# Kernel optimization log

Hardware: AMD Instinct MI355X
Metric: run time of the kernel (lower is better)

The kernel has to match this reference:

```python
import jax, jax.numpy as jnp
import numpy as np

N_NODES = 100000

def gcn_conv(x, edge_index, W, b):
    # normalize=False GCNConv: out[i] = sum_{(j->i) in E} (x W)[j] + b
    h = x @ W                                   # [N, out_dim]
    src, dst = edge_index[0], edge_index[1]
    msgs = h[src]                               # [E, out_dim]
    agg = jax.ops.segment_sum(msgs, dst, num_segments=N_NODES)
    return agg + b

def setup_inputs() -> dict:
    key = jax.random.key(0)
    k1, k2, k3, k4 = jax.random.split(key, 4)
    x = jax.random.normal(k1, (N_NODES, 512), dtype=jnp.float32)
    edge_index = jax.random.randint(k2, (2, 3200000), 0, N_NODES, dtype=jnp.int64)
    W1 = jax.random.normal(k3, (512, 16), dtype=jnp.float32) * (1.0 / np.sqrt(512))
    b1 = jnp.zeros((16,), dtype=jnp.float32)
    W2 = jax.random.normal(k4, (16, 40), dtype=jnp.float32) * (1.0 / np.sqrt(16))
    b2 = jnp.zeros((40,), dtype=jnp.float32)
    return {"x": x, "edge_index": edge_index, "W1": W1, "b1": b1, "W2": W2, "b2": b2}

def reference(x, edge_index, W1, b1, W2, b2):
    h = jax.nn.relu(gcn_conv(x, edge_index, W1, b1))
    # dropout is identity at inference (training=False)
    out = gcn_conv(h, edge_index, W2, b2)
    return jax.nn.log_softmax(out, axis=1)
```

## Files before the change

### kernel.cpp

```cpp
#include <hip/hip_runtime.h>
#include <math.h>

#define N_NODES 100000
#define N_EDGES 3200000
#define BSHIFT 7
#define BNODES 128
#define NB 782
#define PLACE_BLOCKS 400

__global__ __launch_bounds__(256) void gemm1_kernel(
    const float* __restrict__ x, const float* __restrict__ W1,
    float* __restrict__ h, int nrows)
{
    __shared__ float xs[32 * 260];
    const int t = threadIdx.x;
    const int rbase = blockIdx.x * 256;
    const int rq = t >> 2;
    const int cg = t & 3;

    float4 acc0 = make_float4(0.f, 0.f, 0.f, 0.f);
    float4 acc1 = acc0, acc2 = acc0, acc3 = acc0;

    const int kl4  = (t & 7) * 4;
    const int rstg = t >> 3;
    const float4* w4 = (const float4*)W1;

    for (int kc = 0; kc < 512; kc += 32) {
        #pragma unroll
        for (int i = 0; i < 8; ++i) {
            int row = rstg + i * 32;
            int rg  = rbase + row;
            float4 v = make_float4(0.f, 0.f, 0.f, 0.f);
            if (rg < nrows)
                v = *(const float4*)(x + (size_t)rg * 512 + kc + kl4);
            xs[(kl4 + 0) * 260 + row] = v.x;
            xs[(kl4 + 1) * 260 + row] = v.y;
            xs[(kl4 + 2) * 260 + row] = v.z;
            xs[(kl4 + 3) * 260 + row] = v.w;
        }
        __syncthreads();

        #pragma unroll
        for (int k4 = 0; k4 < 8; ++k4) {
            const int k0 = k4 * 4;
            float4 xv0 = *(const float4*)(xs + (k0 + 0) * 260 + rq * 4);
            float4 xv1 = *(const float4*)(xs + (k0 + 1) * 260 + rq * 4);
            float4 xv2 = *(const float4*)(xs + (k0 + 2) * 260 + rq * 4);
            float4 xv3 = *(const float4*)(xs + (k0 + 3) * 260 + rq * 4);
            float4 wv0 = w4[(kc + k0 + 0) * 4 + cg];
            float4 wv1 = w4[(kc + k0 + 1) * 4 + cg];
            float4 wv2 = w4[(kc + k0 + 2) * 4 + cg];
            float4 wv3 = w4[(kc + k0 + 3) * 4 + cg];

            #define GCN_UPD(xv, wv)                                           \
                acc0.x += (xv).x * (wv).x; acc0.y += (xv).x * (wv).y;         \
                acc0.z += (xv).x * (wv).z; acc0.w += (xv).x * (wv).w;         \
                acc1.x += (xv).y * (wv).x; acc1.y += (xv).y * (wv).y;         \
                acc1.z += (xv).y * (wv).z; acc1.w += (xv).y * (wv).w;         \
                acc2.x += (xv).z * (wv).x; acc2.y += (xv).z * (wv).y;         \
                acc2.z += (xv).z * (wv).z; acc2.w += (xv).z * (wv).w;         \
                acc3.x += (xv).w * (wv).x; acc3.y += (xv).w * (wv).y;         \
                acc3.z += (xv).w * (wv).z; acc3.w += (xv).w * (wv).w;
            GCN_UPD(xv0, wv0)
            GCN_UPD(xv1, wv1)
            GCN_UPD(xv2, wv2)
            GCN_UPD(xv3, wv3)
            #undef GCN_UPD
        }
        __syncthreads();
    }
    {
        int rg = rbase + rq * 4;
        if (rg + 0 < nrows) *(float4*)(h + (size_t)(rg + 0) * 16 + cg * 4) = acc0;
        if (rg + 1 < nrows) *(float4*)(h + (size_t)(rg + 1) * 16 + cg * 4) = acc1;
        if (rg + 2 < nrows) *(float4*)(h + (size_t)(rg + 2) * 16 + cg * 4) = acc2;
        if (rg + 3 < nrows) *(float4*)(h + (size_t)(rg + 3) * 16 + cg * 4) = acc3;
    }
}

__global__ __launch_bounds__(256) void bin_count_kernel(
    const int* __restrict__ ei, int* __restrict__ bucket_cnt)
{
    __shared__ int hist[NB];
    const int t = threadIdx.x;
    for (int i = t; i < NB; i += 256) hist[i] = 0;
    __syncthreads();
    const int stride = gridDim.x * 256;
    for (int e = blockIdx.x * 256 + t; e < N_EDGES; e += stride)
        atomicAdd(&hist[ei[N_EDGES + e] >> BSHIFT], 1);
    __syncthreads();
    for (int i = t; i < NB; i += 256)
        if (hist[i]) atomicAdd(&bucket_cnt[i], hist[i]);
}

__global__ __launch_bounds__(1024) void bucket_scan_kernel(
    const int* __restrict__ bucket_cnt, int* __restrict__ bucket_base,
    int* __restrict__ bucket_cursor)
{
    __shared__ int s[1024];
    const int t = threadIdx.x;
    s[t] = (t < NB) ? bucket_cnt[t] : 0;
    __syncthreads();
    for (int off = 1; off < 1024; off <<= 1) {
        int v = (t >= off) ? s[t - off] : 0;
        __syncthreads();
        s[t] += v;
        __syncthreads();
    }
    if (t < NB) {
        int excl = (t == 0) ? 0 : s[t - 1];
        bucket_base[t]   = excl;
        bucket_cursor[t] = excl;
        if (t == NB - 1) bucket_base[NB] = s[t];
    }
}

__global__ __launch_bounds__(256) void bin_place_kernel(
    const int* __restrict__ ei, int* __restrict__ bucket_cursor,
    int* __restrict__ packed)
{
    __shared__ int cnt[NB];
    __shared__ int base_off[NB];
    __shared__ int cur[NB];
    const int t = threadIdx.x;
    const int chunk = (N_EDGES + PLACE_BLOCKS - 1) / PLACE_BLOCKS;
    const int cs = blockIdx.x * chunk;
    const int ce = min(cs + chunk, N_EDGES);

    for (int i = t; i < NB; i += 256) { cnt[i] = 0; cur[i] = 0; }
    __syncthreads();
    for (int e = cs + t; e < ce; e += 256)
        atomicAdd(&cnt[ei[N_EDGES + e] >> BSHIFT], 1);
    __syncthreads();
    for (int i = t; i < NB; i += 256)
        base_off[i] = cnt[i] ? atomicAdd(&bucket_cursor[i], cnt[i]) : 0;
    __syncthreads();
    for (int e = cs + t; e < ce; e += 256) {
        int s = ei[e];
        int d = ei[N_EDGES + e];
        int b = d >> BSHIFT;
        int pos = base_off[b] + atomicAdd(&cur[b], 1);
        packed[pos] = s | ((d & (BNODES - 1)) << 17);
    }
}

__global__ __launch_bounds__(256) void csr_sort_kernel(
    const int* __restrict__ bucket_base, const int* __restrict__ packed,
    int* __restrict__ csr_src, int* __restrict__ row_ptr)
{
    __shared__ int hist[BNODES];
    __shared__ int excl[BNODES];
    __shared__ int cur[BNODES];
    __shared__ int scan[BNODES];
    const int t = threadIdx.x;
    const int b = blockIdx.x;
    if (t < BNODES) { hist[t] = 0; cur[t] = 0; }
    __syncthreads();

    const int bs = bucket_base[b];
    const int be = bucket_base[b + 1];
    for (int e = bs + t; e < be; e += 256)
        atomicAdd(&hist[packed[e] >> 17], 1);
    __syncthreads();

    if (t < BNODES) scan[t] = hist[t];
    __syncthreads();
    for (int off = 1; off < BNODES; off <<= 1) {
        int v = (t < BNODES && t >= off) ? scan[t - off] : 0;
        __syncthreads();
        if (t < BNODES) scan[t] += v;
        __syncthreads();
    }
    if (t < BNODES) {
        int ex = (t == 0) ? 0 : scan[t - 1];
        excl[t] = ex;
        int g = b * BNODES + t;
        if (g < N_NODES) row_ptr[g] = bs + ex;
    }
    if (b == NB - 1 && t == 0) row_ptr[N_NODES] = N_EDGES;
    __syncthreads();

    for (int e = bs + t; e < be; e += 256) {
        int p  = packed[e];
        int dl = p >> 17;
        int pos = bs + excl[dl] + atomicAdd(&cur[dl], 1);
        csr_src[pos] = p & 0x1FFFF;
    }
}

__global__ __launch_bounds__(256) void gather1_kernel(
    const int* __restrict__ row_ptr, const int* __restrict__ csr_src,
    const float* __restrict__ h, const float* __restrict__ b1,
    float* __restrict__ h1)
{
    const int node = (blockIdx.x * 256 + threadIdx.x) >> 6;
    if (node >= N_NODES) return;
    const int lane = threadIdx.x & 63;
    const int c = lane & 15, slot = lane >> 4;
    const int start = row_ptr[node], end = row_ptr[node + 1];

    float acc = 0.f;
    int e = start;
    for (; e + 16 <= end; e += 16) {
        int s0 = csr_src[e + slot * 4 + 0];
        int s1 = csr_src[e + slot * 4 + 1];
        int s2 = csr_src[e + slot * 4 + 2];
        int s3 = csr_src[e + slot * 4 + 3];
        float v0 = h[s0 * 16 + c];
        float v1 = h[s1 * 16 + c];
        float v2 = h[s2 * 16 + c];
        float v3 = h[s3 * 16 + c];
        acc += (v0 + v1) + (v2 + v3);
    }
    for (; e + 4 <= end; e += 4)
        acc += h[csr_src[e + slot] * 16 + c];
    if (e + slot < end)
        acc += h[csr_src[e + slot] * 16 + c];

    acc += __shfl_xor(acc, 16);
    acc += __shfl_xor(acc, 32);
    if (lane < 16)
        h1[(size_t)node * 16 + c] = fmaxf(acc + b1[c], 0.f);
}

__global__ __launch_bounds__(256) void gather2_kernel(
    const int* __restrict__ row_ptr, const int* __restrict__ csr_src,
    const float* __restrict__ h1, const float* __restrict__ W2,
    const float* __restrict__ b2, float* __restrict__ out)
{
    const int node = (blockIdx.x * 256 + threadIdx.x) >> 6;
    if (node >= N_NODES) return;
    const int lane = threadIdx.x & 63;
    const int c = lane & 15, slot = lane >> 4;

    float w2c[16];
    float b2v = 0.f;
    if (lane < 40) {
        b2v = b2[lane];
        #pragma unroll
        for (int k = 0; k < 16; ++k) w2c[k] = W2[k * 40 + lane];
    } else {
        #pragma unroll
        for (int k = 0; k < 16; ++k) w2c[k] = 0.f;
    }

    const int start = row_ptr[node], end = row_ptr[node + 1];
    float acc = 0.f;
    int e = start;
    for (; e + 16 <= end; e += 16) {
        int s0 = csr_src[e + slot * 4 + 0];
        int s1 = csr_src[e + slot * 4 + 1];
        int s2 = csr_src[e + slot * 4 + 2];
        int s3 = csr_src[e + slot * 4 + 3];
        float v0 = h1[s0 * 16 + c];
        float v1 = h1[s1 * 16 + c];
        float v2 = h1[s2 * 16 + c];
        float v3 = h1[s3 * 16 + c];
        acc += (v0 + v1) + (v2 + v3);
    }
    for (; e + 4 <= end; e += 4)
        acc += h1[csr_src[e + slot] * 16 + c];
    if (e + slot < end)
        acc += h1[csr_src[e + slot] * 16 + c];

    acc += __shfl_xor(acc, 16);
    acc += __shfl_xor(acc, 32);

    float z = b2v;
    #pragma unroll
    for (int k = 0; k < 16; ++k)
        z += __shfl(acc, k) * w2c[k];

    float zm = (lane < 40) ? z : -1e30f;
    #pragma unroll
    for (int off = 1; off < 64; off <<= 1)
        zm = fmaxf(zm, __shfl_xor(zm, off));
    float ex = (lane < 40) ? __expf(z - zm) : 0.f;
    float sum = ex;
    #pragma unroll
    for (int off = 1; off < 64; off <<= 1)
        sum += __shfl_xor(sum, off);
    const float lse = zm + __logf(sum);

    if (lane < 40)
        out[(size_t)node * 40 + lane] = z - lse;
}

extern "C" void kernel_launch(void* const* d_in, const int* in_sizes, int n_in,
                              void* d_out, int out_size, void* d_ws, size_t ws_size,
                              hipStream_t stream)
{
    const float* x  = (const float*)d_in[0];
    const int*   ei = (const int*)d_in[1];
    const float* W1 = (const float*)d_in[2];
    const float* b1 = (const float*)d_in[3];
    const float* W2 = (const float*)d_in[4];
    const float* b2 = (const float*)d_in[5];
    float* out = (float*)d_out;

    float* h      = (float*)d_ws;
    int*   csr    = (int*)(h + (size_t)N_NODES * 16);
    int*   packed = csr + N_EDGES;
    float* h1     = (float*)packed;
    int*   rowp   = packed + N_EDGES;
    int*   bcnt   = rowp + (N_NODES + 1);
    int*   bbase  = bcnt + NB;
    int*   bcur   = bbase + (NB + 1);

    const int node_blocks   = (N_NODES + 255) / 256;
    const int gather_blocks = (N_NODES + 3) / 4;

    hipMemsetAsync(bcnt, 0, NB * sizeof(int), stream);
    bin_count_kernel  <<<256, 256, 0, stream>>>(ei, bcnt);
    bucket_scan_kernel<<<1, 1024, 0, stream>>>(bcnt, bbase, bcur);
    bin_place_kernel  <<<PLACE_BLOCKS, 256, 0, stream>>>(ei, bcur, packed);
    csr_sort_kernel   <<<NB, 256, 0, stream>>>(bbase, packed, csr, rowp);

    gemm1_kernel<<<node_blocks, 256, 0, stream>>>(x, W1, h, N_NODES);

    gather1_kernel<<<gather_blocks, 256, 0, stream>>>(rowp, csr, h, b1, h1);
    gather2_kernel<<<gather_blocks, 256, 0, stream>>>(rowp, csr, h1, W2, b2, out);
}
```

Before: 604.6 us.

## Replace shared-memory tiled GEMM1 with per-row shuffle-based register GEMV

```diff
diff --git a/kernel.cpp b/kernel.cpp
--- a/kernel.cpp
+++ b/kernel.cpp
@@ -12,70 +12,42 @@
     const float* __restrict__ x, const float* __restrict__ W1,
     float* __restrict__ h, int nrows)
 {
-    __shared__ float xs[32 * 260];
-    const int t = threadIdx.x;
-    const int rbase = blockIdx.x * 256;
-    const int rq = t >> 2;
-    const int cg = t & 3;
-
-    float4 acc0 = make_float4(0.f, 0.f, 0.f, 0.f);
-    float4 acc1 = acc0, acc2 = acc0, acc3 = acc0;
-
-    const int kl4  = (t & 7) * 4;
-    const int rstg = t >> 3;
+    const int t   = threadIdx.x;
+    const int row = blockIdx.x * 64 + (t >> 2);
+    const int cg  = t & 3;
+    if (row >= nrows) return;
+
     const float4* w4 = (const float4*)W1;
-
-    for (int kc = 0; kc < 512; kc += 32) {
+    const float4* xr = (const float4*)(x + (size_t)row * 512);
+
+    float4 acc = make_float4(0.f, 0.f, 0.f, 0.f);
+
+    for (int kc4 = 0; kc4 < 128; kc4 += 4) {
+        float4 a = xr[kc4 + cg];
         #pragma unroll
-        for (int i = 0; i < 8; ++i) {
-            int row = rstg + i * 32;
-            int rg  = rbase + row;
-            float4 v = make_float4(0.f, 0.f, 0.f, 0.f);
-            if (rg < nrows)
-                v = *(const float4*)(x + (size_t)rg * 512 + kc + kl4);
-            xs[(kl4 + 0) * 260 + row] = v.x;
-            xs[(kl4 + 1) * 260 + row] = v.y;
-            xs[(kl4 + 2) * 260 + row] = v.z;
-            xs[(kl4 + 3) * 260 + row] = v.w;
+        for (int g = 0; g < 4; ++g) {
+            float4 v;
+            v.x = __shfl(a.x, g, 4);
+            v.y = __shfl(a.y, g, 4);
+            v.z = __shfl(a.z, g, 4);
+            v.w = __shfl(a.w, g, 4);
+            const int kb = (kc4 + g) * 4;
+            float4 w0 = w4[(kb + 0) * 4 + cg];
+            float4 w1 = w4[(kb + 1) * 4 + cg];
+            float4 w2 = w4[(kb + 2) * 4 + cg];
+            float4 w3 = w4[(kb + 3) * 4 + cg];
+            acc.x += v.x * w0.x; acc.y += v.x * w0.y;
+            acc.z += v.x * w0.z; acc.w += v.x * w0.w;
+            acc.x += v.y * w1.x; acc.y += v.y * w1.y;
+            acc.z += v.y * w1.z; acc.w += v.y * w1.w;
+            acc.x += v.z * w2.x; acc.y += v.z * w2.y;
+            acc.z += v.z * w2.z; acc.w += v.z * w2.w;
+            acc.x += v.w * w3.x; acc.y += v.w * w3.y;
+            acc.z += v.w * w3.z; acc.w += v.w * w3.w;
         }
-        __syncthreads();
-
-        #pragma unroll
-        for (int k4 = 0; k4 < 8; ++k4) {
-            const int k0 = k4 * 4;
-            float4 xv0 = *(const float4*)(xs + (k0 + 0) * 260 + rq * 4);
-            float4 xv1 = *(const float4*)(xs + (k0 + 1) * 260 + rq * 4);
-            float4 xv2 = *(const float4*)(xs + (k0 + 2) * 260 + rq * 4);
-            float4 xv3 = *(const float4*)(xs + (k0 + 3) * 260 + rq * 4);
-            float4 wv0 = w4[(kc + k0 + 0) * 4 + cg];
-            float4 wv1 = w4[(kc + k0 + 1) * 4 + cg];
-            float4 wv2 = w4[(kc + k0 + 2) * 4 + cg];
-            float4 wv3 = w4[(kc + k0 + 3) * 4 + cg];
-
-            #define GCN_UPD(xv, wv)                                           \
-                acc0.x += (xv).x * (wv).x; acc0.y += (xv).x * (wv).y;         \
-                acc0.z += (xv).x * (wv).z; acc0.w += (xv).x * (wv).w;         \
-                acc1.x += (xv).y * (wv).x; acc1.y += (xv).y * (wv).y;         \
-                acc1.z += (xv).y * (wv).z; acc1.w += (xv).y * (wv).w;         \
-                acc2.x += (xv).z * (wv).x; acc2.y += (xv).z * (wv).y;         \
-                acc2.z += (xv).z * (wv).z; acc2.w += (xv).z * (wv).w;         \
-                acc3.x += (xv).w * (wv).x; acc3.y += (xv).w * (wv).y;         \
-                acc3.z += (xv).w * (wv).z; acc3.w += (xv).w * (wv).w;
-            GCN_UPD(xv0, wv0)
-            GCN_UPD(xv1, wv1)
-            GCN_UPD(xv2, wv2)
-            GCN_UPD(xv3, wv3)
-            #undef GCN_UPD
-        }
-        __syncthreads();
-    }
-    {
-        int rg = rbase + rq * 4;
-        if (rg + 0 < nrows) *(float4*)(h + (size_t)(rg + 0) * 16 + cg * 4) = acc0;
-        if (rg + 1 < nrows) *(float4*)(h + (size_t)(rg + 1) * 16 + cg * 4) = acc1;
-        if (rg + 2 < nrows) *(float4*)(h + (size_t)(rg + 2) * 16 + cg * 4) = acc2;
-        if (rg + 3 < nrows) *(float4*)(h + (size_t)(rg + 3) * 16 + cg * 4) = acc3;
-    }
+    }
+
+    *(float4*)(h + (size_t)row * 16 + cg * 4) = acc;
 }
 
 __global__ __launch_bounds__(256) void bin_count_kernel(
@@ -307,7 +279,7 @@
     int*   bbase  = bcnt + NB;
     int*   bcur   = bbase + (NB + 1);
 
-    const int node_blocks   = (N_NODES + 255) / 256;
+    const int gemm1_blocks  = (N_NODES + 63) / 64;
     const int gather_blocks = (N_NODES + 3) / 4;
 
     hipMemsetAsync(bcnt, 0, NB * sizeof(int), stream);
@@ -316,7 +288,7 @@
     bin_place_kernel  <<<PLACE_BLOCKS, 256, 0, stream>>>(ei, bcur, packed);
     csr_sort_kernel   <<<NB, 256, 0, stream>>>(bbase, packed, csr, rowp);
 
-    gemm1_kernel<<<node_blocks, 256, 0, stream>>>(x, W1, h, N_NODES);
+    gemm1_kernel<<<gemm1_blocks, 256, 0, stream>>>(x, W1, h, N_NODES);
 
     gather1_kernel<<<gather_blocks, 256, 0, stream>>>(rowp, csr, h, b1, h1);
     gather2_kernel<<<gather_blocks, 256, 0, stream>>>(rowp, csr, h1, W2, b2, out);
```

Result: slower. 640.7 us (+6.0%).
